# Kernel tuning notes

Hardware: AMD Instinct MI355X
Metric: run time of the kernel (lower is better)

## Reference

```python
import jax, jax.numpy as jnp
from jax import lax
import numpy as np

K = 31      # avg_pool2d kernel_size
PAD = 15    # avg_pool2d padding
EPS = 1.0
GAMMA = 5.0


def _box_avg(x):
    # Separable 31x31 box filter, stride 1, zero padding 15,
    # count_include_pad=True (PyTorch default) -> always divide by K*K.
    s = lax.reduce_window(x, 0.0, lax.add, (1, 1, K, 1), (1, 1, 1, 1),
                          [(0, 0), (0, 0), (PAD, PAD), (0, 0)])
    s = lax.reduce_window(s, 0.0, lax.add, (1, 1, 1, K), (1, 1, 1, 1),
                          [(0, 0), (0, 0), (0, 0), (PAD, PAD)])
    return s / (K * K)


def setup_inputs() -> dict:
    key = jax.random.key(0)
    k1, k2 = jax.random.split(key)
    shape = (64, 1, 512, 512)  # [B, C, H, W]
    inp = jax.random.uniform(k1, shape, dtype=jnp.float32)
    tgt = jax.random.uniform(k2, shape, dtype=jnp.float32)
    return {"input": inp, "target": tgt}


def reference(input, target):
    weight = 1.0 + GAMMA * jnp.abs(_box_avg(target) - target)
    intersection = jnp.sum(input * target * weight)
    denom = jnp.sum(input * weight) + jnp.sum(target * weight)
    dice = (2.0 * intersection + EPS) / (denom + EPS)
    return 1.0 - dice
```

## Files before the change

### kernel.cpp

```cpp
#include <hip/hip_runtime.h>


#define BATCH 64
#define H     512
#define W     512
#define PADR  15
#define NSEG  64
#define RB    (H / NSEG)
#define NWAVE (BATCH * NSEG)
#define NBLK  (NWAVE / 4)

__global__ __launch_bounds__(256) void fused_kernel(const float* __restrict__ tgt,
                                                    const float* __restrict__ inp,
                                                    float4* __restrict__ partials) {
    const int tid  = threadIdx.x;
    const int lane = tid & 63;
    const int wv   = tid >> 6;
    const int g    = blockIdx.x * 4 + wv;
    const int band = g & (NSEG - 1);
    const int b    = g >> 6;
    const int r0   = band * RB;
    const int col0 = lane * 8;
    const float* timg = tgt + (size_t)b * H * W;
    const float* iimg = inp + (size_t)b * H * W;

    const float mL1 = (lane >= 1) ? 1.f : 0.f;
    const float mR1 = (lane <= 62) ? 1.f : 0.f;
    const float mL2 = (lane >= 2) ? 1.f : 0.f;
    const float mR2 = (lane <= 61) ? 1.f : 0.f;

    float vr[8];
    #pragma unroll
    for (int k = 0; k < 8; ++k) vr[k] = 0.f;
    #pragma unroll
    for (int j = -PADR; j <= PADR; ++j) {
        const int r = r0 + j;
        if (r >= 0 && r < H) {
            const float4 a = *(const float4*)(timg + (size_t)r * W + col0);
            const float4 c = *(const float4*)(timg + (size_t)r * W + col0 + 4);
            vr[0] += a.x; vr[1] += a.y; vr[2] += a.z; vr[3] += a.w;
            vr[4] += c.x; vr[5] += c.y; vr[6] += c.z; vr[7] += c.w;
        }
    }

    const float inv = 1.0f / 961.0f;
    float aI = 0.f, aA = 0.f, aB = 0.f;

    for (int h = r0; h < r0 + RB; ++h) {
        const float p1 = vr[0];
        const float p2 = p1 + vr[1];
        const float p3 = p2 + vr[2];
        const float p4 = p3 + vr[3];
        const float p5 = p4 + vr[4];
        const float p6 = p5 + vr[5];
        const float p7 = p6 + vr[6];
        const float s  = p7 + vr[7];
        const float f1 = s - p1, f2 = s - p2, f3 = s - p3, f4 = s - p4;
        const float f5 = s - p5, f6 = s - p6, f7 = s - p7;

        const float sL1 = __shfl_up(s, 1, 64);
        const float sR1 = __shfl_down(s, 1, 64);
        const float g1 = __shfl_up(f1, 2, 64);
        const float g2 = __shfl_up(f2, 2, 64);
        const float g3 = __shfl_up(f3, 2, 64);
        const float g4 = __shfl_up(f4, 2, 64);
        const float g5 = __shfl_up(f5, 2, 64);
        const float g6 = __shfl_up(f6, 2, 64);
        const float g7 = __shfl_up(f7, 2, 64);
        const float q1 = __shfl_down(p1, 2, 64);
        const float q2 = __shfl_down(p2, 2, 64);
        const float q3 = __shfl_down(p3, 2, 64);
        const float q4 = __shfl_down(p4, 2, 64);
        const float q5 = __shfl_down(p5, 2, 64);
        const float q6 = __shfl_down(p6, 2, 64);
        const float q7 = __shfl_down(p7, 2, 64);

        const float S3 = fmaf(mL1, sL1, fmaf(mR1, sR1, s));
        float win[8];
        win[0] = fmaf(mL2, g1, S3);
        win[1] = fmaf(mL2, g2, fmaf(mR2, q1, S3));
        win[2] = fmaf(mL2, g3, fmaf(mR2, q2, S3));
        win[3] = fmaf(mL2, g4, fmaf(mR2, q3, S3));
        win[4] = fmaf(mL2, g5, fmaf(mR2, q4, S3));
        win[5] = fmaf(mL2, g6, fmaf(mR2, q5, S3));
        win[6] = fmaf(mL2, g7, fmaf(mR2, q6, S3));
        win[7] = fmaf(mR2, q7, S3);

        const float4 t0 = *(const float4*)(timg + (size_t)h * W + col0);
        const float4 t1 = *(const float4*)(timg + (size_t)h * W + col0 + 4);
        const float4 i0 = *(const float4*)(iimg + (size_t)h * W + col0);
        const float4 i1 = *(const float4*)(iimg + (size_t)h * W + col0 + 4);
        const float tv[8] = {t0.x, t0.y, t0.z, t0.w, t1.x, t1.y, t1.z, t1.w};
        const float iv[8] = {i0.x, i0.y, i0.z, i0.w, i1.x, i1.y, i1.z, i1.w};

        #pragma unroll
        for (int j = 0; j < 8; ++j) {
            const float wgt = fmaf(5.0f, fabsf(fmaf(win[j], inv, -tv[j])), 1.0f);
            aI += iv[j] * tv[j] * wgt;
            aA += iv[j] * wgt;
            aB += tv[j] * wgt;
        }

        const int add = h + PADR + 1;
        const int sub = h - PADR;
        if (add < H) {
            const float4 a = *(const float4*)(timg + (size_t)add * W + col0);
            const float4 c = *(const float4*)(timg + (size_t)add * W + col0 + 4);
            vr[0] += a.x; vr[1] += a.y; vr[2] += a.z; vr[3] += a.w;
            vr[4] += c.x; vr[5] += c.y; vr[6] += c.z; vr[7] += c.w;
        }
        if (sub >= 0) {
            const float4 a = *(const float4*)(timg + (size_t)sub * W + col0);
            const float4 c = *(const float4*)(timg + (size_t)sub * W + col0 + 4);
            vr[0] -= a.x; vr[1] -= a.y; vr[2] -= a.z; vr[3] -= a.w;
            vr[4] -= c.x; vr[5] -= c.y; vr[6] -= c.z; vr[7] -= c.w;
        }
    }

    #pragma unroll
    for (int off = 32; off > 0; off >>= 1) {
        aI += __shfl_down(aI, off, 64);
        aA += __shfl_down(aA, off, 64);
        aB += __shfl_down(aB, off, 64);
    }
    __shared__ float part[3][4];
    if (lane == 0) { part[0][wv] = aI; part[1][wv] = aA; part[2][wv] = aB; }
    __syncthreads();
    if (tid == 0) {
        float4 o;
        o.x = part[0][0] + part[0][1] + part[0][2] + part[0][3];
        o.y = part[1][0] + part[1][1] + part[1][2] + part[1][3];
        o.z = part[2][0] + part[2][1] + part[2][2] + part[2][3];
        o.w = 0.f;
        partials[blockIdx.x] = o;
    }
}

__global__ __launch_bounds__(1024) void reduce_kernel(const float4* __restrict__ partials,
                                                      float* __restrict__ out) {
    const int tid = threadIdx.x;
    float aI = 0.f, aA = 0.f, aB = 0.f;
    for (int i = tid; i < NBLK; i += 1024) {
        const float4 v = partials[i];
        aI += v.x; aA += v.y; aB += v.z;
    }
    #pragma unroll
    for (int off = 32; off > 0; off >>= 1) {
        aI += __shfl_down(aI, off, 64);
        aA += __shfl_down(aA, off, 64);
        aB += __shfl_down(aB, off, 64);
    }
    __shared__ float s[3][16];
    const int wvx = tid >> 6, ln = tid & 63;
    if (ln == 0) { s[0][wvx] = aI; s[1][wvx] = aA; s[2][wvx] = aB; }
    __syncthreads();
    if (tid == 0) {
        float I = 0.f, A = 0.f, Bv = 0.f;
        #pragma unroll
        for (int k = 0; k < 16; ++k) { I += s[0][k]; A += s[1][k]; Bv += s[2][k]; }
        out[0] = 1.0f - (2.0f * I + 1.0f) / (A + Bv + 1.0f);
    }
}

extern "C" void kernel_launch(void* const* d_in, const int* in_sizes, int n_in,
                              void* d_out, int out_size, void* d_ws, size_t ws_size,
                              hipStream_t stream) {
    const float* inp = (const float*)d_in[0];
    const float* tgt = (const float*)d_in[1];
    float* out = (float*)d_out;

    float4* partials = (float4*)d_ws;

    fused_kernel<<<NBLK, 256, 0, stream>>>(tgt, inp, partials);
    reduce_kernel<<<1, 1024, 0, stream>>>(partials, out);
}
```

Measured before the change: 175.0 us.

## Stage target rows in an LDS ring buffer shared across four waves

Each block now handles a 64-row band, with its four waves interleaving rows. Target rows sit in a 38-row shared-memory ring buffer that is filled at the start and refilled by register prefetch each step. Window updates and center reads come from LDS instead of re-reading the same global rows several times, which cuts redundant global traffic and halo overlap between bands. The cost is about 76KB of LDS per block, which limits occupancy, plus two barriers per iteration. The reduce kernel shrinks to match 512 partials.

```diff
diff --git a/kernel.cpp b/kernel.cpp
--- a/kernel.cpp
+++ b/kernel.cpp
@@ -5,10 +5,9 @@
 #define H     512
 #define W     512
 #define PADR  15
-#define NSEG  64
-#define RB    (H / NSEG)
-#define NWAVE (BATCH * NSEG)
-#define NBLK  (NWAVE / 4)
+#define RBAND 64
+#define RING  38
+#define NBLK  (BATCH * (H / RBAND))
 
 __global__ __launch_bounds__(256) void fused_kernel(const float* __restrict__ tgt,
                                                     const float* __restrict__ inp,
@@ -16,37 +15,61 @@
     const int tid  = threadIdx.x;
     const int lane = tid & 63;
     const int wv   = tid >> 6;
-    const int g    = blockIdx.x * 4 + wv;
-    const int band = g & (NSEG - 1);
-    const int b    = g >> 6;
-    const int r0   = band * RB;
-    const int col0 = lane * 8;
+    const int blk  = blockIdx.x;
+    const int band = blk & 7;
+    const int b    = blk >> 3;
+    const int R0   = band * RBAND;
     const float* timg = tgt + (size_t)b * H * W;
     const float* iimg = inp + (size_t)b * H * W;
+
+    __shared__ __align__(16) float ring[RING * W];
+
+    #pragma unroll
+    for (int it = 0; it < 19; ++it) {
+        const int u     = tid + it * 256;
+        const int r_off = u >> 7;
+        const int c4    = (u & 127) * 4;
+        const int row   = R0 - 15 + r_off;
+        float4 v = make_float4(0.f, 0.f, 0.f, 0.f);
+        if (row >= 0 && row < H) v = *(const float4*)(timg + (size_t)row * W + c4);
+        *(float4*)&ring[((row + RING) % RING) * W + c4] = v;
+    }
+    __syncthreads();
 
     const float mL1 = (lane >= 1) ? 1.f : 0.f;
     const float mR1 = (lane <= 62) ? 1.f : 0.f;
     const float mL2 = (lane >= 2) ? 1.f : 0.f;
     const float mR2 = (lane <= 61) ? 1.f : 0.f;
+    const int col0 = lane * 8;
 
     float vr[8];
     #pragma unroll
     for (int k = 0; k < 8; ++k) vr[k] = 0.f;
     #pragma unroll
-    for (int j = -PADR; j <= PADR; ++j) {
-        const int r = r0 + j;
-        if (r >= 0 && r < H) {
-            const float4 a = *(const float4*)(timg + (size_t)r * W + col0);
-            const float4 c = *(const float4*)(timg + (size_t)r * W + col0 + 4);
-            vr[0] += a.x; vr[1] += a.y; vr[2] += a.z; vr[3] += a.w;
-            vr[4] += c.x; vr[5] += c.y; vr[6] += c.z; vr[7] += c.w;
-        }
+    for (int jj = -PADR; jj <= PADR; ++jj) {
+        const int rr = R0 + wv + jj;
+        const int sl = ((rr + RING) % RING) * W + col0;
+        const float4 a = *(const float4*)&ring[sl];
+        const float4 c = *(const float4*)&ring[sl + 4];
+        vr[0] += a.x; vr[1] += a.y; vr[2] += a.z; vr[3] += a.w;
+        vr[4] += c.x; vr[5] += c.y; vr[6] += c.z; vr[7] += c.w;
     }
 
     const float inv = 1.0f / 961.0f;
     float aI = 0.f, aA = 0.f, aB = 0.f;
 
-    for (int h = r0; h < r0 + RB; ++h) {
+    for (int j = 0; j < 16; ++j) {
+        const int h = R0 + 4 * j + wv;
+
+        float4 pf0 = make_float4(0.f, 0.f, 0.f, 0.f), pf1 = pf0;
+        const int prow = R0 + 4 * j + 23 + wv;
+        if (j < 14 && prow < H) {
+            pf0 = *(const float4*)(timg + (size_t)prow * W + col0);
+            pf1 = *(const float4*)(timg + (size_t)prow * W + col0 + 4);
+        }
+        const float4 i0 = *(const float4*)(iimg + (size_t)h * W + col0);
+        const float4 i1 = *(const float4*)(iimg + (size_t)h * W + col0 + 4);
+
         const float p1 = vr[0];
         const float p2 = p1 + vr[1];
         const float p3 = p2 + vr[2];
@@ -86,35 +109,43 @@
         win[6] = fmaf(mL2, g7, fmaf(mR2, q6, S3));
         win[7] = fmaf(mR2, q7, S3);
 
-        const float4 t0 = *(const float4*)(timg + (size_t)h * W + col0);
-        const float4 t1 = *(const float4*)(timg + (size_t)h * W + col0 + 4);
-        const float4 i0 = *(const float4*)(iimg + (size_t)h * W + col0);
-        const float4 i1 = *(const float4*)(iimg + (size_t)h * W + col0 + 4);
+        const int slC = (h % RING) * W + col0;
+        const float4 t0 = *(const float4*)&ring[slC];
+        const float4 t1 = *(const float4*)&ring[slC + 4];
         const float tv[8] = {t0.x, t0.y, t0.z, t0.w, t1.x, t1.y, t1.z, t1.w};
         const float iv[8] = {i0.x, i0.y, i0.z, i0.w, i1.x, i1.y, i1.z, i1.w};
 
         #pragma unroll
-        for (int j = 0; j < 8; ++j) {
-            const float wgt = fmaf(5.0f, fabsf(fmaf(win[j], inv, -tv[j])), 1.0f);
-            aI += iv[j] * tv[j] * wgt;
-            aA += iv[j] * wgt;
-            aB += tv[j] * wgt;
-        }
-
-        const int add = h + PADR + 1;
-        const int sub = h - PADR;
-        if (add < H) {
-            const float4 a = *(const float4*)(timg + (size_t)add * W + col0);
-            const float4 c = *(const float4*)(timg + (size_t)add * W + col0 + 4);
-            vr[0] += a.x; vr[1] += a.y; vr[2] += a.z; vr[3] += a.w;
-            vr[4] += c.x; vr[5] += c.y; vr[6] += c.z; vr[7] += c.w;
-        }
-        if (sub >= 0) {
-            const float4 a = *(const float4*)(timg + (size_t)sub * W + col0);
-            const float4 c = *(const float4*)(timg + (size_t)sub * W + col0 + 4);
-            vr[0] -= a.x; vr[1] -= a.y; vr[2] -= a.z; vr[3] -= a.w;
-            vr[4] -= c.x; vr[5] -= c.y; vr[6] -= c.z; vr[7] -= c.w;
-        }
+        for (int k = 0; k < 8; ++k) {
+            const float wgt = fmaf(5.0f, fabsf(fmaf(win[k], inv, -tv[k])), 1.0f);
+            aI += iv[k] * tv[k] * wgt;
+            aA += iv[k] * wgt;
+            aB += tv[k] * wgt;
+        }
+
+        if (j < 15) {
+            #pragma unroll
+            for (int q = 0; q < 4; ++q) {
+                const int slA = ((h + 16 + q) % RING) * W + col0;
+                const int slS = (((h - 15 + q) + RING) % RING) * W + col0;
+                const float4 a0 = *(const float4*)&ring[slA];
+                const float4 a1 = *(const float4*)&ring[slA + 4];
+                const float4 s0 = *(const float4*)&ring[slS];
+                const float4 s1 = *(const float4*)&ring[slS + 4];
+                vr[0] += a0.x - s0.x; vr[1] += a0.y - s0.y;
+                vr[2] += a0.z - s0.z; vr[3] += a0.w - s0.w;
+                vr[4] += a1.x - s1.x; vr[5] += a1.y - s1.y;
+                vr[6] += a1.z - s1.z; vr[7] += a1.w - s1.w;
+            }
+        }
+        __syncthreads();
+
+        if (j < 14) {
+            const int sl = (prow % RING) * W + col0;
+            *(float4*)&ring[sl]     = pf0;
+            *(float4*)&ring[sl + 4] = pf1;
+        }
+        __syncthreads();
     }
 
     #pragma unroll
@@ -123,41 +154,37 @@
         aA += __shfl_down(aA, off, 64);
         aB += __shfl_down(aB, off, 64);
     }
-    __shared__ float part[3][4];
-    if (lane == 0) { part[0][wv] = aI; part[1][wv] = aA; part[2][wv] = aB; }
+    if (lane == 0) { ring[wv] = aI; ring[8 + wv] = aA; ring[16 + wv] = aB; }
     __syncthreads();
     if (tid == 0) {
         float4 o;
-        o.x = part[0][0] + part[0][1] + part[0][2] + part[0][3];
-        o.y = part[1][0] + part[1][1] + part[1][2] + part[1][3];
-        o.z = part[2][0] + part[2][1] + part[2][2] + part[2][3];
+        o.x = ring[0] + ring[1] + ring[2] + ring[3];
+        o.y = ring[8] + ring[9] + ring[10] + ring[11];
+        o.z = ring[16] + ring[17] + ring[18] + ring[19];
         o.w = 0.f;
-        partials[blockIdx.x] = o;
+        partials[blk] = o;
     }
 }
 
-__global__ __launch_bounds__(1024) void reduce_kernel(const float4* __restrict__ partials,
-                                                      float* __restrict__ out) {
+__global__ __launch_bounds__(512) void reduce_kernel(const float4* __restrict__ partials,
+                                                     float* __restrict__ out) {
     const int tid = threadIdx.x;
-    float aI = 0.f, aA = 0.f, aB = 0.f;
-    for (int i = tid; i < NBLK; i += 1024) {
-        const float4 v = partials[i];
-        aI += v.x; aA += v.y; aB += v.z;
-    }
+    const float4 v = partials[tid];
+    float aI = v.x, aA = v.y, aB = v.z;
     #pragma unroll
     for (int off = 32; off > 0; off >>= 1) {
         aI += __shfl_down(aI, off, 64);
         aA += __shfl_down(aA, off, 64);
         aB += __shfl_down(aB, off, 64);
     }
-    __shared__ float s[3][16];
+    __shared__ float s[3][8];
     const int wvx = tid >> 6, ln = tid & 63;
     if (ln == 0) { s[0][wvx] = aI; s[1][wvx] = aA; s[2][wvx] = aB; }
     __syncthreads();
     if (tid == 0) {
         float I = 0.f, A = 0.f, Bv = 0.f;
         #pragma unroll
-        for (int k = 0; k < 16; ++k) { I += s[0][k]; A += s[1][k]; Bv += s[2][k]; }
+        for (int k = 0; k < 8; ++k) { I += s[0][k]; A += s[1][k]; Bv += s[2][k]; }
         out[0] = 1.0f - (2.0f * I + 1.0f) / (A + Bv + 1.0f);
     }
 }
@@ -172,5 +199,5 @@
     float4* partials = (float4*)d_ws;
 
     fused_kernel<<<NBLK, 256, 0, stream>>>(tgt, inp, partials);
-    reduce_kernel<<<1, 1024, 0, stream>>>(partials, out);
+    reduce_kernel<<<1, 512, 0, stream>>>(partials, out);
 }
```

After: 152.0 us. 1.15x faster.
